# Optimization experiments

Measured on AMD Instinct MI355X. Metric: run time of the kernel, lower is better.

The kernel has to match this reference:

```python
import jax, jax.numpy as jnp
import numpy as np

V = 16000      # vocab_size
D = 256        # embedding_dim
H = 512        # hidden_size (bi-LSTM concat)
HD = H // 2    # per-direction hidden
LAB = 32       # labelset_size (30 tags + START/STOP)
T = 512        # seq length
B = 128        # batch
START = 30
STOP = 31
NEG = -10000.0


def setup_inputs() -> dict:
    key = jax.random.key(0)
    ks = jax.random.split(key, 16)
    sc = 0.05
    emb = jax.random.normal(ks[0], (V, D), jnp.float32) * 0.1
    W_ih_f = jax.random.normal(ks[1], (4 * HD, D), jnp.float32) * sc
    W_hh_f = jax.random.normal(ks[2], (4 * HD, HD), jnp.float32) * sc
    b_f = jax.random.normal(ks[3], (4 * HD,), jnp.float32) * sc  # b_ih + b_hh combined
    W_ih_b = jax.random.normal(ks[4], (4 * HD, D), jnp.float32) * sc
    W_hh_b = jax.random.normal(ks[5], (4 * HD, HD), jnp.float32) * sc
    b_b = jax.random.normal(ks[6], (4 * HD,), jnp.float32) * sc
    Wo = jax.random.normal(ks[7], (LAB, H), jnp.float32) * sc
    bo = jnp.zeros((LAB,), jnp.float32)
    transitions = jax.random.normal(ks[8], (LAB, LAB), jnp.float32)
    transitions = transitions.at[STOP, :].set(NEG).at[:, START].set(NEG)
    h0 = jax.random.normal(ks[9], (2, B, HD), jnp.float32)  # init_hidden() uses randn
    c0 = jax.random.normal(ks[10], (2, B, HD), jnp.float32)
    sentences = jax.random.randint(ks[11], (T, B), 0, V, dtype=jnp.int32)
    labels = jax.random.randint(ks[12], (T, B), 0, 30, dtype=jnp.int32)
    masks = jnp.ones((T, B), dtype=bool)
    return {"emb": emb, "W_ih_f": W_ih_f, "W_hh_f": W_hh_f, "b_f": b_f,
            "W_ih_b": W_ih_b, "W_hh_b": W_hh_b, "b_b": b_b,
            "Wo": Wo, "bo": bo, "transitions": transitions,
            "h0": h0, "c0": c0,
            "sentences": sentences, "labels": labels, "masks": masks}


def _lstm_dir(xproj, h0, c0, W_hh):
    # xproj: [T, B, 4*HD] precomputed input projection (+bias)
    def step(carry, xg):
        h, c = carry
        g = xg + h @ W_hh.T
        i, f, gg, o = jnp.split(g, 4, axis=-1)  # torch gate order i,f,g,o
        i = jax.nn.sigmoid(i); f = jax.nn.sigmoid(f)
        gg = jnp.tanh(gg); o = jax.nn.sigmoid(o)
        c = f * c + i * gg
        h = o * jnp.tanh(c)
        return (h, c), h
    _, hs = jax.lax.scan(step, (h0, c0), xproj)
    return hs  # [T, B, HD]


def reference(emb, W_ih_f, W_hh_f, b_f, W_ih_b, W_hh_b, b_b, Wo, bo,
              transitions, h0, c0, sentences, labels, masks):
    # ---- encoder (dropout omitted: eval-mode determinism) ----
    x = emb[sentences]                                   # [T, B, D]
    xf = jnp.einsum('tbd,gd->tbg', x, W_ih_f) + b_f
    hf = _lstm_dir(xf, h0[0], c0[0], W_hh_f)             # [T, B, HD]
    xb = jnp.einsum('tbd,gd->tbg', x, W_ih_b) + b_b
    hb = _lstm_dir(xb[::-1], h0[1], c0[1], W_hh_b)[::-1]
    out = jnp.concatenate([hf, hb], axis=-1)             # [T, B, H]
    feats = jnp.einsum('tbh,lh->tbl', out, Wo) + bo      # [T, B, LAB]

    # ---- CRF forward algorithm (log partition) ----
    dp0 = jnp.full((B, LAB), NEG, jnp.float32).at[:, START].set(0.0)
    def fstep(dp, inp):
        sc, m = inp  # sc: [B, LAB], m: [B]
        new = jax.scipy.special.logsumexp(
            dp[:, :, None] + transitions[None, :, :] + sc[:, None, :], axis=1)
        return jnp.where(m[:, None], new, dp), None
    dpZ, _ = jax.lax.scan(fstep, dp0, (feats, masks))
    Z = jax.scipy.special.logsumexp(dpZ, axis=1)         # [B]

    # ---- gold path score ----
    lab_ext = jnp.concatenate(
        [jnp.full((1, B), START, labels.dtype), labels], axis=0)  # [T+1, B]
    bidx = jnp.arange(B)
    def gstep(dp, inp):
        sc, m, lp, ln = inp
        tmp = dp + transitions[lp, ln] + sc[bidx, ln]
        return jnp.where(m, tmp, dp), None
    gold, _ = jax.lax.scan(gstep, jnp.zeros((B,), jnp.float32),
                           (feats, masks, lab_ext[:-1], lab_ext[1:]))

    return (Z - gold).sum() / B
```

## Files before the change

kernel.cpp:

```cpp
#include <hip/hip_runtime.h>
#include <stdint.h>

typedef __attribute__((ext_vector_type(8))) short short8;
typedef __attribute__((ext_vector_type(4))) float floatx4;
typedef unsigned int u32;
typedef unsigned short u16;
typedef unsigned long long u64;

#define NROW 65536
#define RING 32

#define OFF_TAGS  64
#define OFF_READY 256
#define OFF_WIH   8192
#define OFF_WHH8  1056768
#define OFF_WO    2105344
#define OFF_RING  2138112
#define OFF_OUT   19177472
#define OFF_FE    86286336
#define WS_NEED   94674944

__device__ __forceinline__ u16 f2bf(float f){
  union { float f; u32 u; } v; v.f = f;
  u32 u = v.u;
  return (u16)((u + 0x7FFFu + ((u >> 16) & 1u)) >> 16);
}
__device__ __forceinline__ float bf2f(u16 h){
  union { u32 u; float f; } v; v.u = ((u32)h) << 16; return v.f;
}
__device__ __forceinline__ u32 pack2(float a, float b){
  return (u32)f2bf(a) | ((u32)f2bf(b) << 16);
}
__device__ __forceinline__ u32 pk_fp8x4(float a, float b, float c, float d){
  u32 lo = __builtin_amdgcn_cvt_pk_fp8_f32(a, b, 0, false);
  return (u32)__builtin_amdgcn_cvt_pk_fp8_f32(c, d, lo, true);
}
__device__ __forceinline__ float sigm(float x){
  return __builtin_amdgcn_rcpf(1.f + __expf(-x));
}
__device__ __forceinline__ float tanh_(float x){
  return 1.f - 2.f * __builtin_amdgcn_rcpf(1.f + __expf(2.f * x));
}
__device__ __forceinline__ floatx4 MF(short8 a, short8 b, floatx4 c){
  return __builtin_amdgcn_mfma_f32_16x16x32_bf16(a, b, c, 0, 0, 0);
}
__device__ __forceinline__ floatx4 MF8(long a, long b, floatx4 c){
  return __builtin_amdgcn_mfma_f32_16x16x32_fp8_fp8(a, b, c, 0, 0, 0);
}
__device__ __forceinline__ void ldsload16(const void* g, void* l){
  __builtin_amdgcn_global_load_lds(
      (const __attribute__((address_space(1))) u32*)g,
      (__attribute__((address_space(3))) u32*)l, 16, 0, 17);
}

__global__ void kdiag(float* out, float v){
  if (threadIdx.x == 0 && blockIdx.x == 0) out[0] = v;
}

__global__ void k0(const float* wf, const float* wb, const float* hf, const float* hb,
                   const float* wo, u16* wih, u16* wob, unsigned char* whh8){
  int e = blockIdx.x * 256 + threadIdx.x;
  if (e < 524288){ wih[e] = f2bf(e < 262144 ? wf[e] : wb[e - 262144]); return; }
  if (e < 540672){ wob[e - 524288] = f2bf(wo[e - 524288]); return; }
  if (e < 1064960){
    int t = e - 540672;
    float w = (t < 262144) ? hf[t] : hb[t - 262144];
    whh8[t] = (unsigned char)(__builtin_amdgcn_cvt_pk_fp8_f32(w, w, 0, false) & 0xFF);
  }
}

__launch_bounds__(1024, 4)
__global__ void klstm(const float* emb, const int* sent, const u16* wih,
                      const float* bf_, const float* bb_,
                      const unsigned char* whh8, const float* h0, const float* c0,
                      char* ring, u16* outb, u32* ct, u32* ready){
  __shared__ __align__(16) char SH[98304];
  const int tid = threadIdx.x, w = tid >> 6, l = tid & 63, q = l >> 4, l15 = l & 15;
  const int bid = blockIdx.x;

  if (bid >= 32){
    const int p = bid - 32, dir = p & 1;
    const float* bias = dir ? bb_ : bf_;
    const int m = w & 7, ch = w >> 3;
    int pbud = 1 << 20;
    for (int u = p; u < 1024; u += 224){
      const int s = u >> 1;
      const int t = dir ? 511 - s : s;
      if (s >= 31){
        const int li = l, need = s - 30;
        bool done = false;
        while (!done && pbud > 0){
          int v = need;
          if (li < 16)
            v = (int)__hip_atomic_load(&ct[dir * 16 + li], __ATOMIC_RELAXED, __HIP_MEMORY_SCOPE_AGENT);
          done = (__ballot(v >= need) == ~0ull);
          if (!done){ __builtin_amdgcn_s_sleep(32); pbud--; }
        }
      }
      {
        int r = tid >> 3, g0 = tid & 7;
        const float* er = emb + (size_t)sent[t * 128 + r] * 256;
        #pragma unroll
        for (int j = 0; j < 4; j++){
          int g8 = g0 + j * 8;
          float4 a = *(const float4*)(er + g8 * 8);
          float4 b = *(const float4*)(er + g8 * 8 + 4);
          u32 gg[4] = { pack2(a.x, a.y), pack2(a.z, a.w), pack2(b.x, b.y), pack2(b.z, b.w) };
          *(uint4*)&SH[(g8 * 128 + r) * 16] = *(uint4*)gg;
        }
      }
      __syncthreads();
      short8 Afr[8];
      #pragma unroll
      for (int ks = 0; ks < 8; ks++)
        Afr[ks] = *(const short8*)&SH[((ks * 4 + q) * 128 + m * 16 + l15) * 16];
      char* slot = ring + (size_t)(dir * RING + (s & (RING - 1))) * 262144;
      const int bcw = m * 2 + (q >> 1);
      for (int nt = 0; nt < 16; nt++){
        __syncthreads();
        {
          int r = tid & 63, grp = tid >> 6;
          const u16* wsrc = wih + (size_t)(dir * 1024 + nt * 64 + r) * 256;
          #pragma unroll
          for (int i = 0; i < 2; i++){
            int kg = grp * 2 + i;
            uint4 v = *(const uint4*)(wsrc + kg * 8);
            *(uint4*)&SH[65536 + (kg * 64 + r) * 16] = v;
          }
        }
        __syncthreads();
        floatx4 acc[2];
        acc[0] = floatx4{0.f,0.f,0.f,0.f};
        acc[1] = floatx4{0.f,0.f,0.f,0.f};
        #pragma unroll
        for (int ks = 0; ks < 8; ks++){
          #pragma unroll
          for (int jt = 0; jt < 2; jt++){
            short8 b = *(const short8*)&SH[65536 + ((ks * 4 + q) * 64 + ch * 32 + jt * 16 + l15) * 16];
            acc[jt] = MF(Afr[ks], b, acc[jt]);
          }
        }
        #pragma unroll
        for (int jt = 0; jt < 2; jt++){
          int col = nt * 64 + ch * 32 + jt * 16 + l15;
          float bv = bias[col];
          u32 pr[2] = { pack2(acc[jt][0] + bv, acc[jt][1] + bv),
                        pack2(acc[jt][2] + bv, acc[jt][3] + bv) };
          *(uint2*)(slot + bcw * 16384 + col * 16 + (q & 1) * 8) = *(uint2*)pr;
        }
      }
      asm volatile("s_waitcnt vmcnt(0)" ::: "memory");
      __syncthreads();
      if (tid == 0){
        __builtin_amdgcn_fence(__ATOMIC_RELEASE, "agent");
        __hip_atomic_store(&ready[dir * 512 + s], 1u, __ATOMIC_RELAXED, __HIP_MEMORY_SCOPE_AGENT);
      }
    }
    return;
  }

  const int dir = bid >> 4, bc = bid & 15;
  const int nn = w >> 1, hw = w & 1;
  const int H0 = nn * 32 + hw * 16, hid = H0 + l15;
  const int b0loc = (q & 1) * 4 + (q >> 1) * 2;
  const int i4 = l15 & 3, j4 = l15 >> 2;
  int cbud = 1 << 22;
  const u32 s01 = i4==0?0x00000400u : i4==1?0x00000105u : i4==2?0x06020000u : 0x03070000u;
  const u32 s23 = i4==0?0x04000000u : i4==1?0x01050000u : i4==2?0x00000602u : 0x00000307u;
  const u32 sfn = (i4 < 2) ? 0x07060100u : 0x03020504u;

  long Wf[4][8];
  #pragma unroll
  for (int g = 0; g < 4; g++){
    const unsigned char* wr = whh8 + (size_t)(dir * 1024 + g * 256 + hid) * 256;
    #pragma unroll
    for (int ks = 0; ks < 8; ks++)
      Wf[g][ks] = *(const long*)(wr + ks * 32 + q * 8);
  }
  float creg[2];
  #pragma unroll
  for (int e = 0; e < 2; e++)
    creg[e] = c0[((size_t)dir * 128 + bc * 8 + b0loc + e) * 256 + hid];
  {
    int a = tid * 4;
    int kg = a >> 7, rest = a & 127, b = rest >> 3, off4 = a & 4;
    u32 val0 = 0;
    if (b < 8){
      const float* hr = h0 + ((size_t)dir * 128 + bc * 8 + b) * 256 + kg * 8 + off4;
      val0 = pk_fp8x4(hr[0], hr[1], hr[2], hr[3]);
    }
    *(u32*)&SH[49152 + a] = val0;
    *(u32*)&SH[49152 + 4096 + a] = 0;
  }
  #pragma unroll
  for (int pp = 0; pp < 2; pp++){
    while (__hip_atomic_load(&ready[dir * 512 + pp], __ATOMIC_RELAXED, __HIP_MEMORY_SCOPE_AGENT) == 0u
           && --cbud > 0)
      __builtin_amdgcn_s_sleep(8);
    const char* rp = ring + (size_t)(dir * RING + pp) * 262144 + bc * 16384;
    ldsload16(rp + tid * 16, SH + pp * 16384 + tid * 16);
  }
  u32 rdyv = __hip_atomic_load(&ready[dir * 512 + 2], __ATOMIC_RELAXED, __HIP_MEMORY_SCOPE_AGENT);
  asm volatile("s_waitcnt vmcnt(0)" ::: "memory");
  __syncthreads();

  int xcur = 0, xn2 = 2;
  for (int s = 0; s < 512; s++){
    const int t = dir ? 511 - s : s;
    u32 rdyn = 1u;
    if (s + 3 < 512)
      rdyn = __hip_atomic_load(&ready[dir * 512 + s + 3], __ATOMIC_RELAXED, __HIP_MEMORY_SCOPE_AGENT);
    if (s + 2 < 512){
      if (rdyv == 0u){
        while (__hip_atomic_load(&ready[dir * 512 + s + 2], __ATOMIC_RELAXED, __HIP_MEMORY_SCOPE_AGENT) == 0u
               && --cbud > 0)
          __builtin_amdgcn_s_sleep(2);
      }
      const char* rp = ring + (size_t)(dir * RING + ((s + 2) & (RING - 1))) * 262144 + bc * 16384;
      ldsload16(rp + tid * 16, SH + xn2 * 16384 + tid * 16);
    }
    rdyv = rdyn;

    const char* hb = SH + 49152 + (s & 1) * 4096;
    floatx4 acc[4];
    #pragma unroll
    for (int g = 0; g < 4; g++) acc[g] = floatx4{0.f,0.f,0.f,0.f};
    #pragma unroll
    for (int ks = 0; ks < 8; ks++){
      long Af = *(const long*)(hb + ((ks * 4 + q) * 16 + l15) * 8);
      #pragma unroll
      for (int g = 0; g < 4; g++)
        acc[g] = MF8(Af, Wf[g][ks], acc[g]);
    }

    float v[4][2];
    #pragma unroll
    for (int g = 0; g < 4; g++)
      #pragma unroll
      for (int e = 0; e < 2; e++){
        float hi = __shfl_xor(acc[g][2 + e], 32);
        v[g][e] = (q >= 2) ? hi : acc[g][e];
      }

    const char* xb0 = SH + xcur * 16384;
    u32 xg[4];
    #pragma unroll
    for (int g = 0; g < 4; g++)
      xg[g] = *(const u32*)(xb0 + ((g * 256 + hid) * 16 + b0loc * 2));
    float hv[2];
    #pragma unroll
    for (int e = 0; e < 2; e++){
      float gi = v[0][e] + bf2f((u16)(xg[0] >> (16 * e)));
      float gf = v[1][e] + bf2f((u16)(xg[1] >> (16 * e)));
      float gg = v[2][e] + bf2f((u16)(xg[2] >> (16 * e)));
      float go = v[3][e] + bf2f((u16)(xg[3] >> (16 * e)));
      gi = sigm(gi); gf = sigm(gf); gg = tanh_(gg); go = sigm(go);
      float c = gf * creg[e] + gi * gg;
      creg[e] = c;
      hv[e] = go * tanh_(c);
      outb[((size_t)t * 128 + bc * 8 + b0loc + e) * 512 + dir * 256 + hid] = f2bf(hv[e]);
    }

    {
      u32 pk = (u32)__builtin_amdgcn_cvt_pk_fp8_f32(hv[0], hv[1], 0, false);
      u32 pr = __shfl_xor(pk, 32);
      u32 quad = (q < 2) ? (pk | (pr << 16)) : (pr | (pk << 16));
      u32 r1 = __shfl_xor(quad, 1), r2 = __shfl_xor(quad, 2), r3 = __shfl_xor(quad, 3);
      u32 p01 = __builtin_amdgcn_perm(r1, quad, s01);
      u32 p23 = __builtin_amdgcn_perm(r3, r2, s23);
      u32 outw = __builtin_amdgcn_perm(p23, p01, sfn);
      char* hn = SH + 49152 + ((s + 1) & 1) * 4096;
      if (q < 2){
        int bq = q * 4 + i4;
        int hidg = H0 + j4 * 4;
        *(u32*)&hn[(hidg >> 3) * 128 + bq * 8 + (hidg & 4)] = outw;
      }
    }
    if (tid == 0)
      __hip_atomic_store(&ct[dir * 16 + bc], (u32)(s + 1), __ATOMIC_RELAXED, __HIP_MEMORY_SCOPE_AGENT);

    if (s < 509){
      asm volatile("s_waitcnt vmcnt(4) lgkmcnt(0)" ::: "memory");
      __builtin_amdgcn_s_barrier();
    } else if (s < 511){
      asm volatile("s_waitcnt vmcnt(0)" ::: "memory");
      __syncthreads();
    }
    xcur = (xcur == 2) ? 0 : xcur + 1;
    xn2  = (xn2  == 2) ? 0 : xn2  + 1;
  }
}

__launch_bounds__(256, 2)
__global__ void k5(const u16* outb, const u16* wob, const float* bo, float* fe){
  const int tid = threadIdx.x, w = tid >> 6, l15 = tid & 15, q = (tid >> 4) & 3;
  const int rows0 = blockIdx.x * 64;
  short8 WoF[2][16];
  #pragma unroll
  for (int jt = 0; jt < 2; jt++)
    #pragma unroll
    for (int ks = 0; ks < 16; ks++)
      WoF[jt][ks] = *(const short8*)(wob + (size_t)(jt * 16 + l15) * 512 + ks * 32 + q * 8);
  floatx4 a5[2] = { floatx4{0.f,0.f,0.f,0.f}, floatx4{0.f,0.f,0.f,0.f} };
  const u16* ar = outb + (size_t)(rows0 + w * 16 + l15) * 512;
  #pragma unroll
  for (int ks = 0; ks < 16; ks++){
    short8 a = *(const short8*)(ar + ks * 32 + q * 8);
    a5[0] = MF(a, WoF[0][ks], a5[0]);
    a5[1] = MF(a, WoF[1][ks], a5[1]);
  }
  #pragma unroll
  for (int jt = 0; jt < 2; jt++){
    float bv = bo[jt * 16 + l15];
    #pragma unroll
    for (int rg = 0; rg < 4; rg++)
      fe[(size_t)(rows0 + w * 16 + q * 4 + rg) * 32 + jt * 16 + l15] = a5[jt][rg] + bv;
  }
}

__global__ void k6(const float* fe, const int* labels, const float* trans, float* accp){
  __shared__ float TrL[1024];
  __shared__ __align__(16) float dpL[4][32];
  const int tid = threadIdx.x, w = tid >> 6, l = tid & 63, j = l & 31, half = l >> 5;
  const int b = blockIdx.x * 4 + w;
  for (int i = tid; i < 1024; i += 256) TrL[i] = trans[i];
  __syncthreads();
  float Trl[16];
  #pragma unroll
  for (int ii = 0; ii < 16; ii++) Trl[ii] = TrL[(half * 16 + ii) * 32 + j];
  if (half == 0) dpL[w][j] = (j == 30) ? 0.f : -10000.f;

  float gold = 0.f; int lp = 30;
  float sc = fe[(size_t)b * 32 + j];
  int lab = labels[b];
  float ndF = 0.f;
  for (int t = 0; t < 512; t++){
    float scN = 0.f; int labN = 0;
    if (t < 511){
      scN = fe[((size_t)(t + 1) * 128 + b) * 32 + j];
      labN = labels[(t + 1) * 128 + b];
    }
    float dpv[16], tt[16];
    {
      const float4 a = *(const float4*)&dpL[w][half * 16 + 0];
      const float4 b4 = *(const float4*)&dpL[w][half * 16 + 4];
      const float4 c4 = *(const float4*)&dpL[w][half * 16 + 8];
      const float4 d4 = *(const float4*)&dpL[w][half * 16 + 12];
      dpv[0]=a.x; dpv[1]=a.y; dpv[2]=a.z; dpv[3]=a.w;
      dpv[4]=b4.x; dpv[5]=b4.y; dpv[6]=b4.z; dpv[7]=b4.w;
      dpv[8]=c4.x; dpv[9]=c4.y; dpv[10]=c4.z; dpv[11]=c4.w;
      dpv[12]=d4.x; dpv[13]=d4.y; dpv[14]=d4.z; dpv[15]=d4.w;
    }
    float m = -3.0e38f;
    #pragma unroll
    for (int ii = 0; ii < 16; ii++){ tt[ii] = dpv[ii] + Trl[ii]; m = fmaxf(m, tt[ii]); }
    float M = fmaxf(m, __shfl_xor(m, 32));
    float ssum = 0.f;
    #pragma unroll
    for (int ii = 0; ii < 16; ii++) ssum += __expf(tt[ii] - M);
    ssum += __shfl_xor(ssum, 32);
    float nd = sc + M + __logf(ssum);
    float scl = __shfl(sc, lab);
    gold += TrL[lp * 32 + lab] + scl;
    lp = lab;
    if (half == 0) dpL[w][j] = nd;
    ndF = nd;
    sc = scN; lab = labN;
  }
  float M2 = ndF, S2 = 1.f;
  #pragma unroll
  for (int off = 1; off < 64; off <<= 1){
    float Mo = __shfl_xor(M2, off), So = __shfl_xor(S2, off);
    float Mn = fmaxf(M2, Mo);
    S2 = S2 * __expf(M2 - Mn) + So * __expf(Mo - Mn);
    M2 = Mn;
  }
  float Z = M2 + __logf(S2 * 0.5f);
  if (l == 0) atomicAdd(accp, Z - gold);
}

__global__ void k7(const float* accp, float* out){
  if (threadIdx.x == 0 && blockIdx.x == 0) out[0] = accp[0] * (1.f / 128.f);
}

extern "C" void kernel_launch(void* const* d_in, const int* in_sizes, int n_in,
                              void* d_out, int out_size, void* d_ws, size_t ws_size,
                              hipStream_t stream){
  float* outp = (float*)d_out;
  if (ws_size < (size_t)WS_NEED){
    hipLaunchKernelGGL(kdiag, dim3(1), dim3(64), 0, stream, outp, (float)ws_size);
    return;
  }
  const float* emb  = (const float*)d_in[0];
  const float* Wihf = (const float*)d_in[1];
  const float* Whhf = (const float*)d_in[2];
  const float* bf_  = (const float*)d_in[3];
  const float* Wihb = (const float*)d_in[4];
  const float* Whhb = (const float*)d_in[5];
  const float* bb_  = (const float*)d_in[6];
  const float* Wo   = (const float*)d_in[7];
  const float* bo   = (const float*)d_in[8];
  const float* trans= (const float*)d_in[9];
  const float* h0   = (const float*)d_in[10];
  const float* c0   = (const float*)d_in[11];
  const int*   sent = (const int*)d_in[12];
  const int*   labels = (const int*)d_in[13];

  char* ws = (char*)d_ws;
  float* accp = (float*)ws;
  u32* ct    = (u32*)(ws + OFF_TAGS);
  u32* ready = (u32*)(ws + OFF_READY);
  u16* wih   = (u16*)(ws + OFF_WIH);
  unsigned char* whh8 = (unsigned char*)(ws + OFF_WHH8);
  u16* wob   = (u16*)(ws + OFF_WO);
  char* ring = ws + OFF_RING;
  u16* outb  = (u16*)(ws + OFF_OUT);
  float* fe  = (float*)(ws + OFF_FE);

  hipMemsetAsync(d_ws, 0, 8192, stream);
  hipLaunchKernelGGL(k0, dim3(4160), dim3(256), 0, stream,
                     Wihf, Wihb, Whhf, Whhb, Wo, wih, wob, whh8);
  hipLaunchKernelGGL(klstm, dim3(256), dim3(1024), 0, stream,
                     emb, sent, wih, bf_, bb_, whh8, h0, c0, ring, outb, ct, ready);
  hipLaunchKernelGGL(k5, dim3(1024), dim3(256), 0, stream, outb, wob, bo, fe);
  hipLaunchKernelGGL(k6, dim3(32), dim3(256), 0, stream, fe, labels, trans, accp);
  hipLaunchKernelGGL(k7, dim3(1), dim3(64), 0, stream, accp, outp);
}
```

Baseline: 1.384 ms.

## Restructure LSTM recurrence to 16 batch rows per block with gate-interleaved weights

The recurrent kernel moves from 16 blocks per direction with 8 batch rows each to 8 blocks per direction with 16 batch rows each. W_hh and Wo are permuted at conversion time so each MFMA output holds the four gates (i,f,g,o) for one hidden unit. That lets the input projection seed the accumulator directly and removes the cross-lane shuffles and permutes used to gather gates and rebuild h. The projection producer writes a matching interleaved ring layout, gains 16 more producer blocks, and the progress counter is published every 4 steps instead of every step. The tradeoff is twice the MFMA work and twice the ring data per consumer block, on half as many serial blocks.

```diff
diff --git a/kernel.cpp b/kernel.cpp
--- a/kernel.cpp
+++ b/kernel.cpp
@@ -9,6 +9,7 @@
 
 #define NROW 65536
 #define RING 32
+#define XH 98304
 
 #define OFF_TAGS  64
 #define OFF_READY 256
@@ -20,6 +21,10 @@
 #define OFF_FE    86286336
 #define WS_NEED   94674944
 
+__device__ __forceinline__ int kap(int h){
+  return (h & ~15) | ((h & 3) << 2) | ((h >> 2) & 3);
+}
+
 __device__ __forceinline__ u16 f2bf(float f){
   union { float f; u32 u; } v; v.f = f;
   u32 u = v.u;
@@ -61,10 +66,18 @@
                    const float* wo, u16* wih, u16* wob, unsigned char* whh8){
   int e = blockIdx.x * 256 + threadIdx.x;
   if (e < 524288){ wih[e] = f2bf(e < 262144 ? wf[e] : wb[e - 262144]); return; }
-  if (e < 540672){ wob[e - 524288] = f2bf(wo[e - 524288]); return; }
+  if (e < 540672){
+    int t = e - 524288;
+    int kk = t & 255;
+    wob[t] = f2bf(wo[(t & ~255) | kap(kk)]);
+    return;
+  }
   if (e < 1064960){
     int t = e - 540672;
-    float w = (t < 262144) ? hf[t] : hb[t - 262144];
+    int dir = t >> 18, r = (t >> 8) & 1023, kk = t & 255;
+    int hid = r >> 2, g = r & 3;
+    const float* src = dir ? hb : hf;
+    float w = src[((size_t)(g * 256 + hid)) * 256 + kap(kk)];
     whh8[t] = (unsigned char)(__builtin_amdgcn_cvt_pk_fp8_f32(w, w, 0, false) & 0xFF);
   }
 }
@@ -74,25 +87,25 @@
                       const float* bf_, const float* bb_,
                       const unsigned char* whh8, const float* h0, const float* c0,
                       char* ring, u16* outb, u32* ct, u32* ready){
-  __shared__ __align__(16) char SH[98304];
+  __shared__ __align__(16) char SH[106752];
   const int tid = threadIdx.x, w = tid >> 6, l = tid & 63, q = l >> 4, l15 = l & 15;
   const int bid = blockIdx.x;
 
-  if (bid >= 32){
-    const int p = bid - 32, dir = p & 1;
+  if (bid >= 16){
+    const int p = bid - 16, dir = p & 1;
     const float* bias = dir ? bb_ : bf_;
     const int m = w & 7, ch = w >> 3;
     int pbud = 1 << 20;
-    for (int u = p; u < 1024; u += 224){
+    for (int u = p; u < 1024; u += 240){
       const int s = u >> 1;
       const int t = dir ? 511 - s : s;
-      if (s >= 31){
-        const int li = l, need = s - 30;
+      if (s >= 32){
+        const int li = l, need = s - 31;
         bool done = false;
         while (!done && pbud > 0){
           int v = need;
-          if (li < 16)
-            v = (int)__hip_atomic_load(&ct[dir * 16 + li], __ATOMIC_RELAXED, __HIP_MEMORY_SCOPE_AGENT);
+          if (li < 8)
+            v = (int)__hip_atomic_load(&ct[dir * 8 + li], __ATOMIC_RELAXED, __HIP_MEMORY_SCOPE_AGENT);
           done = (__ballot(v >= need) == ~0ull);
           if (!done){ __builtin_amdgcn_s_sleep(32); pbud--; }
         }
@@ -115,7 +128,6 @@
       for (int ks = 0; ks < 8; ks++)
         Afr[ks] = *(const short8*)&SH[((ks * 4 + q) * 128 + m * 16 + l15) * 16];
       char* slot = ring + (size_t)(dir * RING + (s & (RING - 1))) * 262144;
-      const int bcw = m * 2 + (q >> 1);
       for (int nt = 0; nt < 16; nt++){
         __syncthreads();
         {
@@ -144,9 +156,11 @@
         for (int jt = 0; jt < 2; jt++){
           int col = nt * 64 + ch * 32 + jt * 16 + l15;
           float bv = bias[col];
-          u32 pr[2] = { pack2(acc[jt][0] + bv, acc[jt][1] + bv),
-                        pack2(acc[jt][2] + bv, acc[jt][3] + bv) };
-          *(uint2*)(slot + bcw * 16384 + col * 16 + (q & 1) * 8) = *(uint2*)pr;
+          int g = col >> 8, hid = col & 255;
+          char* basep = slot + m * 32768 + hid * 128 + q * 32 + g * 2;
+          #pragma unroll
+          for (int rg = 0; rg < 4; rg++)
+            *(u16*)(basep + rg * 8) = f2bf(acc[jt][rg] + bv);
         }
       }
       asm volatile("s_waitcnt vmcnt(0)" ::: "memory");
@@ -159,46 +173,35 @@
     return;
   }
 
-  const int dir = bid >> 4, bc = bid & 15;
-  const int nn = w >> 1, hw = w & 1;
-  const int H0 = nn * 32 + hw * 16, hid = H0 + l15;
-  const int b0loc = (q & 1) * 4 + (q >> 1) * 2;
-  const int i4 = l15 & 3, j4 = l15 >> 2;
+  const int dir = bid >> 3, bc = bid & 7;
+  const int b = bc * 16 + l15;
   int cbud = 1 << 22;
-  const u32 s01 = i4==0?0x00000400u : i4==1?0x00000105u : i4==2?0x06020000u : 0x03070000u;
-  const u32 s23 = i4==0?0x04000000u : i4==1?0x01050000u : i4==2?0x00000602u : 0x00000307u;
-  const u32 sfn = (i4 < 2) ? 0x07060100u : 0x03020504u;
 
   long Wf[4][8];
   #pragma unroll
-  for (int g = 0; g < 4; g++){
-    const unsigned char* wr = whh8 + (size_t)(dir * 1024 + g * 256 + hid) * 256;
+  for (int i = 0; i < 4; i++){
+    const unsigned char* wr = whh8 + (size_t)(dir * 1024 + w * 64 + i * 16 + l15) * 256;
     #pragma unroll
     for (int ks = 0; ks < 8; ks++)
-      Wf[g][ks] = *(const long*)(wr + ks * 32 + q * 8);
-  }
-  float creg[2];
-  #pragma unroll
-  for (int e = 0; e < 2; e++)
-    creg[e] = c0[((size_t)dir * 128 + bc * 8 + b0loc + e) * 256 + hid];
+      Wf[i][ks] = *(const long*)(wr + ks * 32 + q * 8);
+  }
+  float creg[4];
+  #pragma unroll
+  for (int i = 0; i < 4; i++)
+    creg[i] = c0[((size_t)dir * 128 + b) * 256 + w * 16 + i * 4 + q];
   {
-    int a = tid * 4;
-    int kg = a >> 7, rest = a & 127, b = rest >> 3, off4 = a & 4;
-    u32 val0 = 0;
-    if (b < 8){
-      const float* hr = h0 + ((size_t)dir * 128 + bc * 8 + b) * 256 + kg * 8 + off4;
-      val0 = pk_fp8x4(hr[0], hr[1], hr[2], hr[3]);
-    }
-    *(u32*)&SH[49152 + a] = val0;
-    *(u32*)&SH[49152 + 4096 + a] = 0;
+    int bb = tid >> 6, k4 = tid & 63;
+    const float* hr = h0 + ((size_t)dir * 128 + bc * 16 + bb) * 256 + (k4 >> 2) * 16 + (k4 & 3);
+    *(u32*)&SH[XH + bb * 264 + k4 * 4] = pk_fp8x4(hr[0], hr[4], hr[8], hr[12]);
   }
   #pragma unroll
   for (int pp = 0; pp < 2; pp++){
     while (__hip_atomic_load(&ready[dir * 512 + pp], __ATOMIC_RELAXED, __HIP_MEMORY_SCOPE_AGENT) == 0u
            && --cbud > 0)
       __builtin_amdgcn_s_sleep(8);
-    const char* rp = ring + (size_t)(dir * RING + pp) * 262144 + bc * 16384;
-    ldsload16(rp + tid * 16, SH + pp * 16384 + tid * 16);
+    const char* rp = ring + (size_t)(dir * RING + pp) * 262144 + bc * 32768;
+    ldsload16(rp + tid * 16, SH + pp * 32768 + tid * 16);
+    ldsload16(rp + 16384 + tid * 16, SH + pp * 32768 + 16384 + tid * 16);
   }
   u32 rdyv = __hip_atomic_load(&ready[dir * 512 + 2], __ATOMIC_RELAXED, __HIP_MEMORY_SCOPE_AGENT);
   asm volatile("s_waitcnt vmcnt(0)" ::: "memory");
@@ -207,6 +210,8 @@
   int xcur = 0, xn2 = 2;
   for (int s = 0; s < 512; s++){
     const int t = dir ? 511 - s : s;
+    if (tid == 0 && (s & 3) == 0)
+      __hip_atomic_store(&ct[dir * 8 + bc], (u32)(s + 1), __ATOMIC_RELAXED, __HIP_MEMORY_SCOPE_AGENT);
     u32 rdyn = 1u;
     if (s + 3 < 512)
       rdyn = __hip_atomic_load(&ready[dir * 512 + s + 3], __ATOMIC_RELAXED, __HIP_MEMORY_SCOPE_AGENT);
@@ -216,68 +221,48 @@
                && --cbud > 0)
           __builtin_amdgcn_s_sleep(2);
       }
-      const char* rp = ring + (size_t)(dir * RING + ((s + 2) & (RING - 1))) * 262144 + bc * 16384;
-      ldsload16(rp + tid * 16, SH + xn2 * 16384 + tid * 16);
+      const char* rp = ring + (size_t)(dir * RING + ((s + 2) & (RING - 1))) * 262144 + bc * 32768;
+      char* xb = SH + xn2 * 32768;
+      ldsload16(rp + tid * 16, xb + tid * 16);
+      ldsload16(rp + 16384 + tid * 16, xb + 16384 + tid * 16);
     }
     rdyv = rdyn;
 
-    const char* hb = SH + 49152 + (s & 1) * 4096;
+    const char* xb0 = SH + xcur * 32768;
     floatx4 acc[4];
     #pragma unroll
-    for (int g = 0; g < 4; g++) acc[g] = floatx4{0.f,0.f,0.f,0.f};
+    for (int i = 0; i < 4; i++){
+      u64 xg = *(const u64*)(xb0 + ((w * 16 + i * 4 + q) * 16 + l15) * 8);
+      acc[i][0] = bf2f((u16)xg);
+      acc[i][1] = bf2f((u16)(xg >> 16));
+      acc[i][2] = bf2f((u16)(xg >> 32));
+      acc[i][3] = bf2f((u16)(xg >> 48));
+    }
+    const char* hbuf = SH + XH + (s & 1) * 4224;
     #pragma unroll
     for (int ks = 0; ks < 8; ks++){
-      long Af = *(const long*)(hb + ((ks * 4 + q) * 16 + l15) * 8);
+      long Bf = *(const long*)(hbuf + l15 * 264 + ks * 32 + q * 8);
       #pragma unroll
-      for (int g = 0; g < 4; g++)
-        acc[g] = MF8(Af, Wf[g][ks], acc[g]);
-    }
-
-    float v[4][2];
-    #pragma unroll
-    for (int g = 0; g < 4; g++)
-      #pragma unroll
-      for (int e = 0; e < 2; e++){
-        float hi = __shfl_xor(acc[g][2 + e], 32);
-        v[g][e] = (q >= 2) ? hi : acc[g][e];
-      }
-
-    const char* xb0 = SH + xcur * 16384;
-    u32 xg[4];
-    #pragma unroll
-    for (int g = 0; g < 4; g++)
-      xg[g] = *(const u32*)(xb0 + ((g * 256 + hid) * 16 + b0loc * 2));
-    float hv[2];
-    #pragma unroll
-    for (int e = 0; e < 2; e++){
-      float gi = v[0][e] + bf2f((u16)(xg[0] >> (16 * e)));
-      float gf = v[1][e] + bf2f((u16)(xg[1] >> (16 * e)));
-      float gg = v[2][e] + bf2f((u16)(xg[2] >> (16 * e)));
-      float go = v[3][e] + bf2f((u16)(xg[3] >> (16 * e)));
-      gi = sigm(gi); gf = sigm(gf); gg = tanh_(gg); go = sigm(go);
-      float c = gf * creg[e] + gi * gg;
-      creg[e] = c;
-      hv[e] = go * tanh_(c);
-      outb[((size_t)t * 128 + bc * 8 + b0loc + e) * 512 + dir * 256 + hid] = f2bf(hv[e]);
-    }
-
+      for (int i = 0; i < 4; i++)
+        acc[i] = MF8(Wf[i][ks], Bf, acc[i]);
+    }
+    float hv[4];
+    #pragma unroll
+    for (int i = 0; i < 4; i++){
+      float gi = sigm(acc[i][0]);
+      float gf = sigm(acc[i][1]);
+      float gg = tanh_(acc[i][2]);
+      float go = sigm(acc[i][3]);
+      float c = gf * creg[i] + gi * gg;
+      creg[i] = c;
+      hv[i] = go * tanh_(c);
+    }
     {
-      u32 pk = (u32)__builtin_amdgcn_cvt_pk_fp8_f32(hv[0], hv[1], 0, false);
-      u32 pr = __shfl_xor(pk, 32);
-      u32 quad = (q < 2) ? (pk | (pr << 16)) : (pr | (pk << 16));
-      u32 r1 = __shfl_xor(quad, 1), r2 = __shfl_xor(quad, 2), r3 = __shfl_xor(quad, 3);
-      u32 p01 = __builtin_amdgcn_perm(r1, quad, s01);
-      u32 p23 = __builtin_amdgcn_perm(r3, r2, s23);
-      u32 outw = __builtin_amdgcn_perm(p23, p01, sfn);
-      char* hn = SH + 49152 + ((s + 1) & 1) * 4096;
-      if (q < 2){
-        int bq = q * 4 + i4;
-        int hidg = H0 + j4 * 4;
-        *(u32*)&hn[(hidg >> 3) * 128 + bq * 8 + (hidg & 4)] = outw;
-      }
-    }
-    if (tid == 0)
-      __hip_atomic_store(&ct[dir * 16 + bc], (u32)(s + 1), __ATOMIC_RELAXED, __HIP_MEMORY_SCOPE_AGENT);
+      u32 pr[2] = { pack2(hv[0], hv[1]), pack2(hv[2], hv[3]) };
+      *(uint2*)(outb + ((size_t)t * 128 + b) * 512 + dir * 256 + w * 16 + q * 4) = *(uint2*)pr;
+    }
+    *(u32*)&SH[XH + ((s + 1) & 1) * 4224 + l15 * 264 + w * 16 + q * 4] =
+        pk_fp8x4(hv[0], hv[1], hv[2], hv[3]);
 
     if (s < 509){
       asm volatile("s_waitcnt vmcnt(4) lgkmcnt(0)" ::: "memory");
```

After: 2.107 ms. +52.2%, slower.
